# Kernel tuning notes

Hardware: AMD Instinct MI355X
Metric: run time of the kernel (lower is better)

The kernel has to match this reference:

```python
import jax, jax.numpy as jnp
import numpy as np

B, D_MODEL, H, D_MEM, M = 512, 2048, 8, 128, 512
MAX_WRITE_FACTOR = 0.7


def act(x):
    # elu(x) + 1, the standard positive linear-attention kernel activation
    return jax.nn.elu(x) + 1.0


def setup_inputs() -> dict:
    key = jax.random.key(0)
    ks = jax.random.split(key, 9)
    s = 1.0 / np.sqrt(D_MODEL)
    return {
        "key": jax.random.normal(ks[0], (B, D_MODEL), jnp.float32),
        "values": jax.random.normal(ks[1], (B, D_MODEL), jnp.float32),
        "memories": jax.random.normal(ks[2], (B, M, D_MEM), jnp.float32),
        "write_mass": jax.random.uniform(ks[3], (B, M, D_MEM), jnp.float32),
        "batch_mask": jnp.zeros((B,), jnp.bool_),
        "W_key": jax.random.normal(ks[4], (D_MODEL, H * D_MEM), jnp.float32) * s,
        "b_key": jnp.zeros((H * D_MEM,), jnp.float32),
        "W_val": jax.random.normal(ks[5], (D_MODEL, 2 * H * D_MEM), jnp.float32) * s,
        "b_val": jnp.zeros((2 * H * D_MEM,), jnp.float32),
        "addresses": jax.random.normal(ks[6], (M, D_MEM), jnp.float32),
        "interpolation_logits": jax.random.normal(ks[7], (M, D_MEM), jnp.float32),
    }


def reference(key, values, memories, write_mass, batch_mask,
              W_key, b_key, W_val, b_val, addresses, interpolation_logits):
    # project write heads
    k = (key @ W_key + b_key).reshape(B, H, D_MEM)            # (B, H, Dm)
    v = (values @ W_val + b_val).reshape(B, H, 2 * D_MEM)     # (B, H, 2Dm)

    # linear attention kernel over heads (items = H)
    ak = act(k)
    matrix = jnp.einsum('bhd,bhe->bde', ak, v)                 # (B, Dm, 2Dm)
    normalizer = jnp.sum(ak, axis=1)                           # (B, Dm)

    # read with memory addresses as queries
    aq = act(addresses)                                        # (M, Dm)
    numerator = jnp.einsum('md,bde->bme', aq, matrix)          # (B, M, 2Dm)
    denominator = jnp.einsum('md,bd->bm', aq, normalizer) + 1e-5
    results = numerator / denominator[..., None]

    update = results[..., :D_MEM]                              # (B, M, Dm)
    write_logits = results[..., D_MEM:]                        # (B, M, Dm)

    write_probability = jax.nn.sigmoid(write_logits)
    interpolation_factor = jax.nn.sigmoid(interpolation_logits)  # (M, Dm)
    write_factor = MAX_WRITE_FACTOR * write_probability * interpolation_factor

    # probability-gated EMA-style commit
    next_memories = memories * (1.0 - write_factor) + update * write_factor
    next_mass = write_mass + write_factor

    mask = batch_mask[:, None, None]
    next_memories = jnp.where(mask, memories, next_memories)
    next_mass = jnp.where(mask, write_mass, next_mass)
    return next_memories, next_mass
```

## Files before the change

kernel.cpp:

```cpp
#include <hip/hip_runtime.h>


typedef _Float16 half8  __attribute__((ext_vector_type(8)));
typedef _Float16 half4v __attribute__((ext_vector_type(4)));
typedef float    f32x4  __attribute__((ext_vector_type(4)));

#define NB      512
#define DMODEL  2048
#define NH      8
#define DMEM    128
#define NM      512
#define NMTOT   33554432

__device__ __forceinline__ f32x4 ntload4(const float* p) {
    return __builtin_nontemporal_load((const f32x4*)p);
}
__device__ __forceinline__ void ntstore4(float* p, f32x4 v) {
    __builtin_nontemporal_store(v, (f32x4*)p);
}

__global__ void cvt_f32_f16(const float* __restrict__ in, _Float16* __restrict__ out, int n4) {
    int i = blockIdx.x * blockDim.x + threadIdx.x;
    if (i < n4) {
        float4 v = ((const float4*)in)[i];
        half4v o;
        o[0] = (_Float16)v.x; o[1] = (_Float16)v.y;
        o[2] = (_Float16)v.z; o[3] = (_Float16)v.w;
        ((half4v*)out)[i] = o;
    }
}

__global__ void transp_cvt(const float* __restrict__ W, _Float16* __restrict__ Wt, int N) {
    __shared__ float tile[32][33];
    const int k0 = blockIdx.x * 32, n0 = blockIdx.y * 32;
    const int c = threadIdx.x & 31, r0 = threadIdx.x >> 5;
#pragma unroll
    for (int i = 0; i < 4; i++) {
        int r = r0 + i * 8;
        tile[r][c] = W[(size_t)(k0 + r) * N + n0 + c];
    }
    __syncthreads();
#pragma unroll
    for (int i = 0; i < 4; i++) {
        int r = r0 + i * 8;
        Wt[(size_t)(n0 + r) * 2048 + k0 + c] = (_Float16)tile[c][r];
    }
}

__global__ void prep_aq(const float* __restrict__ addresses, const float* __restrict__ ilog,
                        float* __restrict__ aqF, _Float16* __restrict__ aqH,
                        float* __restrict__ sigI) {
    int i = blockIdx.x * 256 + threadIdx.x;
    float a = addresses[i];
    float v = a > 0.f ? a + 1.f : __expf(a);
    aqF[i] = v;
    aqH[i] = (_Float16)v;
    sigI[i] = 1.0f / (1.0f + __expf(-ilog[i]));
}

__global__ __launch_bounds__(256) void gemm_kv(
        const _Float16* __restrict__ key16,
        const _Float16* __restrict__ val16,
        const _Float16* __restrict__ WkT,
        const _Float16* __restrict__ WvT,
        const float* __restrict__ b_key,
        const float* __restrict__ b_val,
        float* __restrict__ akF,
        _Float16* __restrict__ vH) {
    __shared__ _Float16 As[2][64][72];
    __shared__ _Float16 Bs[2][64][72];

    const int t = threadIdx.x;
    const int m0 = blockIdx.x * 64;
    const int n0 = blockIdx.y * 64;
    const bool isK = (n0 < 1024);
    const _Float16* aSrc = isK ? key16 : val16;
    const _Float16* bSrc = isK ? (WkT + (size_t)n0 * 2048)
                               : (WvT + (size_t)(n0 - 1024) * 2048);

    const int w = t >> 6, lane = t & 63;
    const int col = lane & 15, q = lane >> 4;
    const int wm = (w & 1) * 32, wn = (w >> 1) * 32;

    const int row0 = t >> 3, ch = t & 7;
    const int row1 = (t + 256) >> 3;

    f32x4 acc[2][2];
#pragma unroll
    for (int i = 0; i < 2; i++)
#pragma unroll
        for (int j = 0; j < 2; j++) acc[i][j] = (f32x4){0.f, 0.f, 0.f, 0.f};

    uint4 ra0 = *(const uint4*)(aSrc + (size_t)(m0 + row0) * 2048 + ch * 8);
    uint4 ra1 = *(const uint4*)(aSrc + (size_t)(m0 + row1) * 2048 + ch * 8);
    uint4 rb0 = *(const uint4*)(bSrc + (size_t)row0 * 2048 + ch * 8);
    uint4 rb1 = *(const uint4*)(bSrc + (size_t)row1 * 2048 + ch * 8);

    int buf = 0;
    for (int k0 = 0; k0 < 2048; k0 += 64) {
        *(uint4*)&As[buf][row0][ch * 8] = ra0;
        *(uint4*)&As[buf][row1][ch * 8] = ra1;
        *(uint4*)&Bs[buf][row0][ch * 8] = rb0;
        *(uint4*)&Bs[buf][row1][ch * 8] = rb1;
        if (k0 + 64 < 2048) {
            const int kn = k0 + 64;
            ra0 = *(const uint4*)(aSrc + (size_t)(m0 + row0) * 2048 + kn + ch * 8);
            ra1 = *(const uint4*)(aSrc + (size_t)(m0 + row1) * 2048 + kn + ch * 8);
            rb0 = *(const uint4*)(bSrc + (size_t)row0 * 2048 + kn + ch * 8);
            rb1 = *(const uint4*)(bSrc + (size_t)row1 * 2048 + kn + ch * 8);
        }
        __syncthreads();
#pragma unroll
        for (int ks = 0; ks < 2; ks++) {
            half8 a0 = *(const half8*)&As[buf][wm + col][ks * 32 + q * 8];
            half8 a1 = *(const half8*)&As[buf][wm + 16 + col][ks * 32 + q * 8];
            half8 b0 = *(const half8*)&Bs[buf][wn + col][ks * 32 + q * 8];
            half8 b1 = *(const half8*)&Bs[buf][wn + 16 + col][ks * 32 + q * 8];
            acc[0][0] = __builtin_amdgcn_mfma_f32_16x16x32_f16(a0, b0, acc[0][0], 0, 0, 0);
            acc[0][1] = __builtin_amdgcn_mfma_f32_16x16x32_f16(a0, b1, acc[0][1], 0, 0, 0);
            acc[1][0] = __builtin_amdgcn_mfma_f32_16x16x32_f16(a1, b0, acc[1][0], 0, 0, 0);
            acc[1][1] = __builtin_amdgcn_mfma_f32_16x16x32_f16(a1, b1, acc[1][1], 0, 0, 0);
        }
        buf ^= 1;
    }
#pragma unroll
    for (int mt = 0; mt < 2; mt++) {
#pragma unroll
        for (int nt = 0; nt < 2; nt++) {
            int n = n0 + wn + nt * 16 + col;
#pragma unroll
            for (int r = 0; r < 4; r++) {
                int m = m0 + wm + mt * 16 + q * 4 + r;
                float x = acc[mt][nt][r];
                if (isK) {
                    x += b_key[n];
                    akF[(size_t)m * 1024 + n] = (x > 0.f) ? (x + 1.f) : __expf(x);
                } else {
                    int nn = n - 1024;
                    x += b_val[nn];
                    vH[(size_t)m * 2048 + nn] = (_Float16)x;
                }
            }
        }
    }
}

__global__ __launch_bounds__(1024, 1) void fused_mem(
    const float* __restrict__ akF,
    const _Float16* __restrict__ vH,
    const _Float16* __restrict__ aqH,
    const float* __restrict__ aqF,
    const float* __restrict__ sigI,
    const float* __restrict__ memories,
    const float* __restrict__ write_mass,
    const unsigned char* __restrict__ bmask,
    float* __restrict__ out) {
    __shared__ _Float16 matT[256][DMEM + 8];
    __shared__ float    xtile[16][16][40];
    __shared__ float    sA[NH][DMEM];
    __shared__ _Float16 sV[NH][256];
    __shared__ float    sNrm[DMEM];
    __shared__ float    sDen[NM];

    const int b = blockIdx.x;
    const int t = threadIdx.x;
    const int w = t >> 6, lane = t & 63;
    const int col = lane & 15, q = lane >> 4;

    if (t < 256) {
        ((float4*)&sA[0][0])[t] = ((const float4*)(akF + (size_t)b * 1024))[t];
        ((uint4*)&sV[0][0])[t]  = ((const uint4*)(vH + (size_t)b * 2048))[t];
    }
    __syncthreads();

    if (t < 128) {
        float s = 0.f;
#pragma unroll
        for (int h = 0; h < NH; h++) s += sA[h][t];
        sNrm[t] = s;
    }

    {
        const int d0 = (t & 31) * 4;
        const int e0 = (t >> 5) * 8;
        float c[8][4];
#pragma unroll
        for (int e = 0; e < 8; e++)
#pragma unroll
            for (int d = 0; d < 4; d++) c[e][d] = 0.f;
#pragma unroll
        for (int h = 0; h < NH; h++) {
            float4 av = *(const float4*)&sA[h][d0];
            half8 vv = *(const half8*)&sV[h][e0];
#pragma unroll
            for (int e = 0; e < 8; e++) {
                float vf = (float)vv[e];
                c[e][0] += av.x * vf; c[e][1] += av.y * vf;
                c[e][2] += av.z * vf; c[e][3] += av.w * vf;
            }
        }
#pragma unroll
        for (int e = 0; e < 8; e++) {
            half4v o;
            o[0] = (_Float16)c[e][0]; o[1] = (_Float16)c[e][1];
            o[2] = (_Float16)c[e][2]; o[3] = (_Float16)c[e][3];
            *(half4v*)&matT[e0 + e][d0] = o;
        }
    }
    __syncthreads();

    {
        const int l32 = lane & 31;
        const int hh = lane >> 5;
        const float4 nv = *(const float4*)&sNrm[l32 * 4];
#pragma unroll 4
        for (int pass = 0; pass < 16; pass++) {
            int m = pass * 32 + w * 2 + hh;
            float4 qv = *(const float4*)(aqF + (size_t)m * 128 + l32 * 4);
            float s = qv.x * nv.x + qv.y * nv.y + qv.z * nv.z + qv.w * nv.w;
            s += __shfl_xor(s, 1);  s += __shfl_xor(s, 2);  s += __shfl_xor(s, 4);
            s += __shfl_xor(s, 8);  s += __shfl_xor(s, 16);
            if (l32 == 0) sDen[m] = 1.0f / (s + 1e-5f);
        }
    }
    __syncthreads();

    const float wfscale = (bmask[b] != 0) ? 0.0f : 0.7f;
    const size_t obase = (size_t)b * (NM * DMEM);
    float (*tile)[40] = xtile[w];
    const int slice = w & 3;
    const int eg0 = 32 * slice + (lane & 3) * 4;
    const int mloc = lane >> 2;

    for (int it = 0; it < 2; it++) {
        const int mbase = ((w >> 2) + it * 4) * 64;
        f32x4 acc[4][4];
#pragma unroll
        for (int i = 0; i < 4; i++)
#pragma unroll
            for (int j = 0; j < 4; j++) acc[i][j] = (f32x4){0.f, 0.f, 0.f, 0.f};

#pragma unroll
        for (int ks = 0; ks < 4; ks++) {
            half8 bfr[4];
#pragma unroll
            for (int nt = 0; nt < 4; nt++) {
                int eb = 32 * slice + (nt & 1) * 16 + (nt >> 1) * 128;
                bfr[nt] = *(const half8*)&matT[eb + col][ks * 32 + q * 8];
            }
#pragma unroll
            for (int mt = 0; mt < 4; mt++) {
                const half8 af = *(const half8*)(aqH + (size_t)(mbase + mt * 16 + col) * 128
                                                 + ks * 32 + q * 8);
#pragma unroll
                for (int nt = 0; nt < 4; nt++)
                    acc[mt][nt] = __builtin_amdgcn_mfma_f32_16x16x32_f16(af, bfr[nt],
                                                                         acc[mt][nt], 0, 0, 0);
            }
        }

#pragma unroll
        for (int mt = 0; mt < 4; mt++) {
#pragma unroll
            for (int r = 0; r < 4; r++) {
                tile[q * 4 + r][col]      = acc[mt][0][r];
                tile[q * 4 + r][16 + col] = acc[mt][1][r];
            }
            __builtin_amdgcn_wave_barrier();
            f32x4 u0 = *(const f32x4*)&tile[mloc][(lane & 3) * 4];
            f32x4 u1 = *(const f32x4*)&tile[mloc][(lane & 3) * 4 + 16];
            __builtin_amdgcn_wave_barrier();
#pragma unroll
            for (int r = 0; r < 4; r++) {
                tile[q * 4 + r][col]      = acc[mt][2][r];
                tile[q * 4 + r][16 + col] = acc[mt][3][r];
            }
            __builtin_amdgcn_wave_barrier();
            f32x4 g0 = *(const f32x4*)&tile[mloc][(lane & 3) * 4];
            f32x4 g1 = *(const f32x4*)&tile[mloc][(lane & 3) * 4 + 16];
            __builtin_amdgcn_wave_barrier();

            const int mglob = mbase + mt * 16 + mloc;
            const float rc = sDen[mglob];
#pragma unroll
            for (int cch = 0; cch < 2; cch++) {
                const int eg = eg0 + cch * 16;
                const size_t gi = obase + (size_t)mglob * 128 + eg;
                const f32x4 u = cch ? u1 : u0;
                const f32x4 g = cch ? g1 : g0;
                const f32x4 mem = ntload4(memories + gi);
                const f32x4 wms = ntload4(write_mass + gi);
                const f32x4 si  = *(const f32x4*)(sigI + (size_t)mglob * 128 + eg);
                f32x4 o1, o2;
#pragma unroll
                for (int j = 0; j < 4; j++) {
                    const float upd = u[j] * rc;
                    const float wl  = g[j] * rc;
                    const float wpb = 1.0f / (1.0f + __expf(-wl));
                    const float wf  = wfscale * wpb * si[j];
                    o1[j] = mem[j] + wf * (upd - mem[j]);
                    o2[j] = wms[j] + wf;
                }
                ntstore4(out + gi, o1);
                ntstore4(out + NMTOT + gi, o2);
            }
        }
    }
}

extern "C" void kernel_launch(void* const* d_in, const int* in_sizes, int n_in,
                              void* d_out, int out_size, void* d_ws, size_t ws_size,
                              hipStream_t stream) {
    const float* key        = (const float*)d_in[0];
    const float* values     = (const float*)d_in[1];
    const float* memories   = (const float*)d_in[2];
    const float* write_mass = (const float*)d_in[3];
    const unsigned char* bm = (const unsigned char*)d_in[4];
    const float* W_key      = (const float*)d_in[5];
    const float* b_key      = (const float*)d_in[6];
    const float* W_val      = (const float*)d_in[7];
    const float* b_val      = (const float*)d_in[8];
    const float* addresses  = (const float*)d_in[9];
    const float* ilog       = (const float*)d_in[10];
    float* out = (float*)d_out;

    char* ws = (char*)d_ws;
    _Float16* key16 = (_Float16*)ws;  ws += (size_t)512 * 2048 * 2;
    _Float16* val16 = (_Float16*)ws;  ws += (size_t)512 * 2048 * 2;
    _Float16* WkT   = (_Float16*)ws;  ws += (size_t)1024 * 2048 * 2;
    _Float16* WvT   = (_Float16*)ws;  ws += (size_t)2048 * 2048 * 2;
    float*    akF   = (float*)ws;     ws += (size_t)512 * 1024 * 4;
    _Float16* vH    = (_Float16*)ws;  ws += (size_t)512 * 2048 * 2;
    float*    aqF   = (float*)ws;     ws += (size_t)512 * 128 * 4;
    _Float16* aqH   = (_Float16*)ws;  ws += (size_t)512 * 128 * 2;
    float*    sigI  = (float*)ws;     ws += (size_t)512 * 128 * 4;

    cvt_f32_f16<<<1024, 256, 0, stream>>>(key, key16, 262144);
    cvt_f32_f16<<<1024, 256, 0, stream>>>(values, val16, 262144);
    transp_cvt<<<dim3(64, 32), 256, 0, stream>>>(W_key, WkT, 1024);
    transp_cvt<<<dim3(64, 64), 256, 0, stream>>>(W_val, WvT, 2048);
    prep_aq<<<256, 256, 0, stream>>>(addresses, ilog, aqF, aqH, sigI);
    gemm_kv<<<dim3(8, 48), 256, 0, stream>>>(key16, val16, WkT, WvT, b_key, b_val, akF, vH);
    fused_mem<<<512, 1024, 0, stream>>>(akF, vH, aqH, aqF, sigI, memories, write_mass, bm, out);
}
```

Before: 627.1 us.

## Software-pipeline memory/mass loads across 16-row steps with block-wide transpose tiles

Restructures the read/commit phase of fused_mem into 8 steps of 16 rows per wave, and double-buffers the memories, write_mass and sigmoid-interpolation loads one step ahead in registers. The first prefetch is issued before the shared-memory setup. The per-wave transpose tile is replaced by block-wide uT/gT tiles synchronized with s_barrier, so each thread writes a contiguous 128-float row segment. The aim is to hide HBM latency of the streaming loads behind the MFMA work. In exchange it adds two block barriers per step and more register pressure from the prefetch buffers.

```diff
diff --git a/kernel.cpp b/kernel.cpp
--- a/kernel.cpp
+++ b/kernel.cpp
@@ -145,6 +145,8 @@
     }
 }
 
+struct PFBuf { f32x4 pm[2]; f32x4 pw[2]; f32x4 ps[2]; };
+
 __global__ __launch_bounds__(1024, 1) void fused_mem(
     const float* __restrict__ akF,
     const _Float16* __restrict__ vH,
@@ -156,7 +158,8 @@
     const unsigned char* __restrict__ bmask,
     float* __restrict__ out) {
     __shared__ _Float16 matT[256][DMEM + 8];
-    __shared__ float    xtile[16][16][40];
+    __shared__ float    uT[64][132];
+    __shared__ float    gT[64][132];
     __shared__ float    sA[NH][DMEM];
     __shared__ _Float16 sV[NH][256];
     __shared__ float    sNrm[DMEM];
@@ -166,6 +169,24 @@
     const int t = threadIdx.x;
     const int w = t >> 6, lane = t & 63;
     const int col = lane & 15, q = lane >> 4;
+    const int wq = w >> 2, slice = w & 3;
+    const int lr = lane >> 5, e4 = (lane & 31) * 4;
+    const size_t obase = (size_t)b * (NM * DMEM);
+
+    PFBuf A, B;
+
+    auto pf_issue = [&](PFBuf& pb, int s) {
+        const int mrow = (wq + (s >> 2) * 4) * 64 + (s & 3) * 16 + slice * 4 + lr;
+#pragma unroll
+        for (int p = 0; p < 2; p++) {
+            const size_t gi = (size_t)(mrow + p * 2) * 128 + e4;
+            pb.pm[p] = ntload4(memories + obase + gi);
+            pb.pw[p] = ntload4(write_mass + obase + gi);
+            pb.ps[p] = *(const f32x4*)(sigI + gi);
+        }
+    };
+
+    pf_issue(A, 0);
 
     if (t < 256) {
         ((float4*)&sA[0][0])[t] = ((const float4*)(akF + (size_t)b * 1024))[t];
@@ -226,85 +247,70 @@
     __syncthreads();
 
     const float wfscale = (bmask[b] != 0) ? 0.0f : 0.7f;
-    const size_t obase = (size_t)b * (NM * DMEM);
-    float (*tile)[40] = xtile[w];
-    const int slice = w & 3;
-    const int eg0 = 32 * slice + (lane & 3) * 4;
-    const int mloc = lane >> 2;
-
-    for (int it = 0; it < 2; it++) {
-        const int mbase = ((w >> 2) + it * 4) * 64;
-        f32x4 acc[4][4];
-#pragma unroll
-        for (int i = 0; i < 4; i++)
-#pragma unroll
-            for (int j = 0; j < 4; j++) acc[i][j] = (f32x4){0.f, 0.f, 0.f, 0.f};
-
+
+    auto do_step = [&](int s, PFBuf& cur, PFBuf& nxt) {
+        if (s < 7) pf_issue(nxt, s + 1);
+
+        const int mrowBase = (wq + (s >> 2) * 4) * 64 + (s & 3) * 16;
+        f32x4 acc[4];
+#pragma unroll
+        for (int nt = 0; nt < 4; nt++) acc[nt] = (f32x4){0.f, 0.f, 0.f, 0.f};
 #pragma unroll
         for (int ks = 0; ks < 4; ks++) {
-            half8 bfr[4];
+            const half8 af = *(const half8*)(aqH + (size_t)(mrowBase + col) * 128
+                                             + ks * 32 + q * 8);
 #pragma unroll
             for (int nt = 0; nt < 4; nt++) {
-                int eb = 32 * slice + (nt & 1) * 16 + (nt >> 1) * 128;
-                bfr[nt] = *(const half8*)&matT[eb + col][ks * 32 + q * 8];
+                const half8 bf = *(const half8*)&matT[slice * 32 + (nt & 1) * 16
+                                                      + (nt >> 1) * 128 + col]
+                                                     [ks * 32 + q * 8];
+                acc[nt] = __builtin_amdgcn_mfma_f32_16x16x32_f16(af, bf, acc[nt], 0, 0, 0);
             }
-#pragma unroll
-            for (int mt = 0; mt < 4; mt++) {
-                const half8 af = *(const half8*)(aqH + (size_t)(mbase + mt * 16 + col) * 128
-                                                 + ks * 32 + q * 8);
-#pragma unroll
-                for (int nt = 0; nt < 4; nt++)
-                    acc[mt][nt] = __builtin_amdgcn_mfma_f32_16x16x32_f16(af, bfr[nt],
-                                                                         acc[mt][nt], 0, 0, 0);
+        }
+
+        asm volatile("s_waitcnt lgkmcnt(0)" ::: "memory");
+        __builtin_amdgcn_s_barrier();
+        __builtin_amdgcn_sched_barrier(0);
+
+        const int r0 = wq * 16 + q * 4;
+#pragma unroll
+        for (int r = 0; r < 4; r++) {
+            uT[r0 + r][slice * 32 + col]      = acc[0][r];
+            uT[r0 + r][slice * 32 + 16 + col] = acc[1][r];
+            gT[r0 + r][slice * 32 + col]      = acc[2][r];
+            gT[r0 + r][slice * 32 + 16 + col] = acc[3][r];
+        }
+
+        asm volatile("s_waitcnt lgkmcnt(0)" ::: "memory");
+        __builtin_amdgcn_s_barrier();
+        __builtin_amdgcn_sched_barrier(0);
+
+#pragma unroll
+        for (int p = 0; p < 2; p++) {
+            const int row = w * 4 + p * 2 + lr;
+            const int m = mrowBase + slice * 4 + p * 2 + lr;
+            const f32x4 u = *(const f32x4*)&uT[row][e4];
+            const f32x4 g = *(const f32x4*)&gT[row][e4];
+            const float rc = sDen[m];
+            const size_t gi = obase + (size_t)m * 128 + e4;
+            f32x4 o1, o2;
+#pragma unroll
+            for (int j = 0; j < 4; j++) {
+                const float upd = u[j] * rc;
+                const float wl  = g[j] * rc;
+                const float wpb = 1.0f / (1.0f + __expf(-wl));
+                const float wf  = wfscale * wpb * cur.ps[p][j];
+                o1[j] = cur.pm[p][j] + wf * (upd - cur.pm[p][j]);
+                o2[j] = cur.pw[p][j] + wf;
             }
-        }
-
-#pragma unroll
-        for (int mt = 0; mt < 4; mt++) {
-#pragma unroll
-            for (int r = 0; r < 4; r++) {
-                tile[q * 4 + r][col]      = acc[mt][0][r];
-                tile[q * 4 + r][16 + col] = acc[mt][1][r];
-            }
-            __builtin_amdgcn_wave_barrier();
-            f32x4 u0 = *(const f32x4*)&tile[mloc][(lane & 3) * 4];
-            f32x4 u1 = *(const f32x4*)&tile[mloc][(lane & 3) * 4 + 16];
-            __builtin_amdgcn_wave_barrier();
-#pragma unroll
-            for (int r = 0; r < 4; r++) {
-                tile[q * 4 + r][col]      = acc[mt][2][r];
-                tile[q * 4 + r][16 + col] = acc[mt][3][r];
-            }
-            __builtin_amdgcn_wave_barrier();
-            f32x4 g0 = *(const f32x4*)&tile[mloc][(lane & 3) * 4];
-            f32x4 g1 = *(const f32x4*)&tile[mloc][(lane & 3) * 4 + 16];
-            __builtin_amdgcn_wave_barrier();
-
-            const int mglob = mbase + mt * 16 + mloc;
-            const float rc = sDen[mglob];
-#pragma unroll
-            for (int cch = 0; cch < 2; cch++) {
-                const int eg = eg0 + cch * 16;
-                const size_t gi = obase + (size_t)mglob * 128 + eg;
-                const f32x4 u = cch ? u1 : u0;
-                const f32x4 g = cch ? g1 : g0;
-                const f32x4 mem = ntload4(memories + gi);
-                const f32x4 wms = ntload4(write_mass + gi);
-                const f32x4 si  = *(const f32x4*)(sigI + (size_t)mglob * 128 + eg);
-                f32x4 o1, o2;
-#pragma unroll
-                for (int j = 0; j < 4; j++) {
-                    const float upd = u[j] * rc;
-                    const float wl  = g[j] * rc;
-                    const float wpb = 1.0f / (1.0f + __expf(-wl));
-                    const float wf  = wfscale * wpb * si[j];
-                    o1[j] = mem[j] + wf * (upd - mem[j]);
-                    o2[j] = wms[j] + wf;
-                }
-                ntstore4(out + gi, o1);
-                ntstore4(out + NMTOT + gi, o2);
-            }
-        }
+            ntstore4(out + gi, o1);
+            ntstore4(out + NMTOT + gi, o2);
+        }
+    };
+
+    for (int s2 = 0; s2 < 8; s2 += 2) {
+        do_step(s2,     A, B);
+        do_step(s2 + 1, B, A);
     }
 }
 
```

Measured after the change: 544.0 us. 1.15x faster.
